# Optimization experiments

Measured on AMD Instinct MI355X. Metric: run time of the kernel, lower is better.

Reference implementation:

```python
import jax, jax.numpy as jnp
import numpy as np

EMB = 2048; H = 32; G = 8; D = 64; GS = H // G; EPS = 1e-6

def _rmsnorm(x, scale):
    x32 = x.astype(jnp.float32)
    var = jnp.mean(x32 * x32, axis=-1, keepdims=True)
    return (x32 * jax.lax.rsqrt(var + EPS) * scale).astype(x.dtype)

def _rope(x, cos, sin):
    # x: [B, h, S, D]; cos/sin: [S, D]
    d = x.shape[-1]
    x1, x2 = x[..., : d // 2], x[..., d // 2 :]
    rot = jnp.concatenate([-x2, x1], axis=-1)
    return (x * cos[None, None] + rot * sin[None, None]).astype(x.dtype)

def setup_inputs() -> dict:
    key = jax.random.key(0)
    ks = jax.random.split(key, 6)
    B, S = 2, 2048
    x = jax.random.normal(ks[0], (B, S, EMB), jnp.float32)
    # causal mask: True = blocked (masked_fill semantics)
    mask = jnp.triu(jnp.ones((S, S), dtype=bool), k=1)
    # standard RoPE tables, half-dim rotation, shape [S, D]
    inv_freq = 1.0 / (10000.0 ** (jnp.arange(0, D, 2, dtype=jnp.float32) / D))
    ang = jnp.arange(S, dtype=jnp.float32)[:, None] * inv_freq[None, :]  # [S, D/2]
    cos = jnp.concatenate([jnp.cos(ang), jnp.cos(ang)], axis=-1)
    sin = jnp.concatenate([jnp.sin(ang), jnp.sin(ang)], axis=-1)
    Wq = jax.random.normal(ks[1], (EMB, H * D), jnp.float32) * 0.02
    Wk = jax.random.normal(ks[2], (EMB, G * D), jnp.float32) * 0.02
    Wv = jax.random.normal(ks[3], (EMB, G * D), jnp.float32) * 0.02
    Wo = jax.random.normal(ks[4], (H * D, EMB), jnp.float32) * 0.02
    q_scale = jnp.ones((D,), jnp.float32)
    k_scale = jnp.ones((D,), jnp.float32)
    return {"x": x, "mask": mask, "cos": cos, "sin": sin, "Wq": Wq, "Wk": Wk,
            "Wv": Wv, "Wo": Wo, "q_scale": q_scale, "k_scale": k_scale}

def reference(x, mask, cos, sin, Wq, Wk, Wv, Wo, q_scale, k_scale):
    B, S, _ = x.shape
    q = (x @ Wq).reshape(B, S, H, D).transpose(0, 2, 1, 3)  # [B,H,S,D]
    k = (x @ Wk).reshape(B, S, G, D).transpose(0, 2, 1, 3)  # [B,G,S,D]
    v = (x @ Wv).reshape(B, S, G, D).transpose(0, 2, 1, 3)
    q = _rmsnorm(q, q_scale)
    k = _rmsnorm(k, k_scale)
    q = _rope(q, cos, sin)
    k = _rope(k, cos, sin)
    # GQA expansion (repeat_interleave over head dim)
    k = jnp.repeat(k, GS, axis=1)
    v = jnp.repeat(v, GS, axis=1)
    scale = 1.0 / np.float32(np.sqrt(D))
    s = jnp.einsum('bhqd,bhkd->bhqk', q.astype(jnp.float32), k.astype(jnp.float32)) * scale
    # flash path is causal regardless of `mask` arg; mask here equals causal
    s = jnp.where(mask[None, None], -jnp.inf, s)
    w = jax.nn.softmax(s, axis=-1)
    ctx = jnp.einsum('bhqk,bhkd->bhqd', w, v.astype(jnp.float32))
    ctx = ctx.transpose(0, 2, 1, 3).reshape(B, S, H * D)
    return ctx @ Wo
```

## Files before the change

### kernel.cpp

```cpp
#include <hip/hip_runtime.h>
#include <hip/hip_bf16.h>
#include <cstdint>
#include <cstddef>

#define EMB   2048
#define NH_   32
#define NG_   8
#define DH_   64
#define SEQ_  2048
#define BB_   2
#define MTOT  4096
#define LDQKV 3072

typedef __attribute__((ext_vector_type(8))) short s16x8;
typedef __attribute__((ext_vector_type(8))) unsigned short u16x8;
typedef __attribute__((ext_vector_type(4))) float f32x4;
typedef __attribute__((ext_vector_type(16))) float f32x16;
typedef __attribute__((ext_vector_type(4))) unsigned int u32x4;
typedef __attribute__((ext_vector_type(2))) unsigned int u32x2;
typedef __attribute__((ext_vector_type(2))) int i32x2;

__device__ __forceinline__ float bf2f(unsigned short u) {
  unsigned int x = (unsigned int)u << 16; return __uint_as_float(x);
}
__device__ __forceinline__ unsigned short f2bf(float f) {
  unsigned int x = __float_as_uint(f);
  x = x + 0x7FFFu + ((x >> 16) & 1u);
  return (unsigned short)(x >> 16);
}
__device__ __forceinline__ float ninf() { return __int_as_float(0xff800000); }
__device__ __forceinline__ unsigned int pack_bf2(float a, float b) {
  unsigned int r;
  asm("v_cvt_pk_bf16_f32 %0, %1, %2" : "=v"(r) : "v"(a), "v"(b));
  return r;
}
__device__ __forceinline__ void plswap(unsigned int& a, unsigned int& b) {
  i32x2 r = __builtin_amdgcn_permlane32_swap((int)a, (int)b, false, false);
  a = (unsigned int)r[0]; b = (unsigned int)r[1];
}
__device__ __forceinline__ void plswapf(float& a, float& b) {
  unsigned int ua = __float_as_uint(a), ub = __float_as_uint(b);
  plswap(ua, ub);
  a = __uint_as_float(ua); b = __uint_as_float(ub);
}

__device__ __forceinline__ void glds16(const void* g, void* l) {
  __builtin_amdgcn_global_load_lds((const __attribute__((address_space(1))) void*)g,
                                   (__attribute__((address_space(3))) void*)l, 16, 0, 0);
}

__global__ __launch_bounds__(256)
void cvtx(const float* __restrict__ x, unsigned short* __restrict__ xb) {
  size_t i = (size_t)blockIdx.x * 256 + threadIdx.x;
  float4 a = *(const float4*)(x + i * 8);
  float4 c = *(const float4*)(x + i * 8 + 4);
  u16x8 o;
  o[0] = f2bf(a.x); o[1] = f2bf(a.y); o[2] = f2bf(a.z); o[3] = f2bf(a.w);
  o[4] = f2bf(c.x); o[5] = f2bf(c.y); o[6] = f2bf(c.z); o[7] = f2bf(c.w);
  *(u16x8*)(xb + i * 8) = o;
}

__global__ __launch_bounds__(256)
void wtrans(const float* __restrict__ in, unsigned short* __restrict__ out, int N) {
  __shared__ float tile[64][65];
  const int tid = threadIdx.x;
  const int n0 = blockIdx.x * 64, k0 = blockIdx.y * 64;
  #pragma unroll
  for (int jj = 0; jj < 4; ++jj) {
    int r = (tid >> 4) + jj * 16;
    int c = (tid & 15) * 4;
    float4 v = *(const float4*)(in + (size_t)(k0 + r) * N + n0 + c);
    tile[r][c] = v.x; tile[r][c + 1] = v.y; tile[r][c + 2] = v.z; tile[r][c + 3] = v.w;
  }
  __syncthreads();
  #pragma unroll
  for (int rep = 0; rep < 2; ++rep) {
    int u = rep * 256 + tid;
    int nl = u >> 3, ch = u & 7;
    u16x8 o;
    #pragma unroll
    for (int e = 0; e < 8; ++e) o[e] = f2bf(tile[ch * 8 + e][nl]);
    *(u16x8*)(out + (size_t)(n0 + nl) * 2048 + k0 + ch * 8) = o;
  }
}

template<int BF16OUT>
__global__ __launch_bounds__(256)
void gemm_bt(const unsigned short* __restrict__ A, const unsigned short* __restrict__ Bt,
             void* __restrict__ C, int ldc) {
  __shared__ __align__(16) unsigned short As[128 * 32];
  __shared__ __align__(16) unsigned short Bs[128 * 32];
  const int tid = threadIdx.x;
  const int w = tid >> 6, lane = tid & 63;
  const int grp = lane >> 4, l15 = lane & 15;
  const int wr = w >> 1, wc = w & 1;
  const int bm = blockIdx.y * 128, bn = blockIdx.x * 128;
  f32x4 acc[4][4] = {};
  for (int k0 = 0; k0 < 2048; k0 += 32) {
    #pragma unroll
    for (int j = 0; j < 2; ++j) {
      int unit = (j * 4 + w) * 64 + lane;
      int row = unit >> 2, ch = unit & 3;
      glds16(A  + (size_t)(bm + row) * 2048 + k0 + ch * 8, (char*)As + (j * 4 + w) * 1024);
      glds16(Bt + (size_t)(bn + row) * 2048 + k0 + ch * 8, (char*)Bs + (j * 4 + w) * 1024);
    }
    __syncthreads();
    s16x8 af[4], bf[4];
    #pragma unroll
    for (int i = 0; i < 4; ++i)
      af[i] = *(const s16x8*)((const char*)As + (wr * 64 + i * 16 + l15) * 64 + grp * 16);
    #pragma unroll
    for (int j = 0; j < 4; ++j)
      bf[j] = *(const s16x8*)((const char*)Bs + (wc * 64 + j * 16 + l15) * 64 + grp * 16);
    #pragma unroll
    for (int i = 0; i < 4; ++i)
      #pragma unroll
      for (int j = 0; j < 4; ++j)
        acc[i][j] = __builtin_amdgcn_mfma_f32_16x16x32_bf16(af[i], bf[j], acc[i][j], 0, 0, 0);
    __syncthreads();
  }
  #pragma unroll
  for (int i = 0; i < 4; ++i)
    #pragma unroll
    for (int j = 0; j < 4; ++j)
      #pragma unroll
      for (int r = 0; r < 4; ++r) {
        int row = bm + wr * 64 + i * 16 + grp * 4 + r;
        int col = bn + wc * 64 + j * 16 + l15;
        float v = acc[i][j][r];
        if (BF16OUT) ((unsigned short*)C)[(size_t)row * ldc + col] = f2bf(v);
        else         ((float*)C)[(size_t)row * ldc + col] = v;
      }
}

__global__ __launch_bounds__(256)
void rmsrope(unsigned short* __restrict__ t, const float* __restrict__ scale,
             const float* __restrict__ cs, const float* __restrict__ sn, int coff, float post) {
  int m = blockIdx.x * 4 + (threadIdx.x >> 6);
  int h = blockIdx.y;
  int lane = threadIdx.x & 63;
  int spos = m & (SEQ_ - 1);
  unsigned short* p = t + (size_t)m * LDQKV + coff + h * 64 + lane;
  float val = bf2f(*p);
  float sq = val * val;
  #pragma unroll
  for (int off = 32; off; off >>= 1) sq += __shfl_xor(sq, off);
  float r = rsqrtf(sq * (1.f / 64.f) + 1e-6f);
  float xn = val * r * scale[lane];
  float partner = __shfl_xor(xn, 32);
  float c = cs[spos * 64 + lane], s = sn[spos * 64 + lane];
  float o = (lane < 32) ? (xn * c - partner * s) : fmaf(xn, c, partner * s);
  *p = f2bf(o * post);
}

__global__ __launch_bounds__(256)
void kvtile(const unsigned short* __restrict__ qkv, unsigned short* __restrict__ Kt,
            unsigned short* __restrict__ Vt) {
  __shared__ unsigned short Kl[32][72];
  __shared__ unsigned short Vl[32][72];
  const int tid = threadIdx.x;
  const int kt = blockIdx.x;
  const int bg = blockIdx.y;
  const int b = bg >> 3, g = bg & 7;
  {
    int row = tid >> 3, ch = tid & 7;
    u16x8 kv = *(const u16x8*)(qkv + (size_t)(b * SEQ_ + kt * 32 + row) * LDQKV + 2048 + g * 64 + ch * 8);
    #pragma unroll
    for (int e = 0; e < 8; ++e) Kl[row][ch * 8 + e] = kv[e];
    u16x8 vv = *(const u16x8*)(qkv + (size_t)(b * SEQ_ + kt * 32 + row) * LDQKV + 2560 + g * 64 + ch * 8);
    #pragma unroll
    for (int e = 0; e < 8; ++e) Vl[row][ch * 8 + e] = vv[e];
  }
  __syncthreads();
  {
    int c = tid >> 5, row = tid & 31;
    u16x8 o;
    #pragma unroll
    for (int e = 0; e < 8; ++e) o[e] = Kl[row][c * 8 + e];
    *(u16x8*)(Kt + (((size_t)(bg * 64 + kt)) << 11) + (c * 32 + row) * 8) = o;
  }
  {
    int c = tid >> 6, d = tid & 63;
    u16x8 o;
    #pragma unroll
    for (int e = 0; e < 8; ++e) o[e] = Vl[c * 8 + e][d];
    *(u16x8*)(Vt + (((size_t)(bg * 64 + kt)) << 11) + (c * 64 + d) * 8) = o;
  }
}

__global__ __launch_bounds__(256)
void attn_mfma9(const unsigned short* __restrict__ qkv, const unsigned short* __restrict__ Ktg,
                const unsigned short* __restrict__ Vtg, unsigned short* __restrict__ ctx) {
  __shared__ __align__(16) unsigned short LA[8 * 1024];
  __shared__ __align__(16) unsigned short LB[8 * 1024];
  const int tid = threadIdx.x;
  const int w = tid >> 6, lane = tid & 63;
  const int l31 = lane & 31, half = lane >> 5;
  const int bid = blockIdx.x;
  const int x8 = bid & 7, r = bid >> 3;
  const int bg = x8 + 8 * (r & 1);
  const int rr = r >> 1;
  const int slot = rr >> 4, gi = rr & 15;
  const int qt = (slot == 0) ? (63 - gi) : (slot == 1) ? gi
               : (slot == 2) ? (47 - gi) : (16 + gi);
  const int b = bg >> 3, g = bg & 7, h = g * 4 + w;
  const int qbase = qt * 32;
  const int nkt = qt + 1;
  const int nit = (nkt + 1) >> 1;

  s16x8 qf[4];
  #pragma unroll
  for (int s = 0; s < 4; ++s)
    qf[s] = *(const s16x8*)(qkv + (size_t)(b * SEQ_ + qbase + l31) * LDQKV + h * 64 + half * 8 + s * 16);

  f32x16 acc0 = {}, acc1 = {};
  float l_st = 0.f;

  const size_t tbase = ((size_t)(bg * 64)) << 11;
  const int soff = (w << 9) + lane * 8;

  auto stage = [&](unsigned short* Lb, int pi) {
    const int kt0 = 2 * pi, kt1 = 2 * pi + 1;
    glds16(Ktg + tbase + ((size_t)kt0 << 11) + soff, (char*)Lb + (w << 10));
    glds16(Vtg + tbase + ((size_t)kt0 << 11) + soff, (char*)Lb + 8192 + (w << 10));
    if (kt1 < nkt) {
      glds16(Ktg + tbase + ((size_t)kt1 << 11) + soff, (char*)Lb + 4096 + (w << 10));
      glds16(Vtg + tbase + ((size_t)kt1 << 11) + soff, (char*)Lb + 12288 + (w << 10));
    }
  };

  auto sub = [&](const char* Kb, const char* Vb, bool diag, float& lsum) {
    s16x8 KF0 = *(const s16x8*)(Kb + (((0 + half) << 5) + l31) * 16);
    s16x8 KF1 = *(const s16x8*)(Kb + (((2 + half) << 5) + l31) * 16);
    s16x8 KF2 = *(const s16x8*)(Kb + (((4 + half) << 5) + l31) * 16);
    s16x8 KF3 = *(const s16x8*)(Kb + (((6 + half) << 5) + l31) * 16);
    s16x8 vf00 = *(const s16x8*)(Vb + (((half) << 6) + l31) * 16);
    s16x8 vf01 = *(const s16x8*)(Vb + (((2 + half) << 6) + l31) * 16);
    s16x8 vf10 = *(const s16x8*)(Vb + (((half) << 6) + 32 + l31) * 16);
    s16x8 vf11 = *(const s16x8*)(Vb + (((2 + half) << 6) + 32 + l31) * 16);
    f32x16 st = {};
    __builtin_amdgcn_s_setprio(1);
    st = __builtin_amdgcn_mfma_f32_32x32x16_bf16(KF0, qf[0], st, 0, 0, 0);
    st = __builtin_amdgcn_mfma_f32_32x32x16_bf16(KF1, qf[1], st, 0, 0, 0);
    st = __builtin_amdgcn_mfma_f32_32x32x16_bf16(KF2, qf[2], st, 0, 0, 0);
    st = __builtin_amdgcn_mfma_f32_32x32x16_bf16(KF3, qf[3], st, 0, 0, 0);
    __builtin_amdgcn_s_setprio(0);
    if (diag) {
      #pragma unroll
      for (int r2 = 0; r2 < 16; ++r2) {
        int key = (r2 & 3) + 8 * (r2 >> 2) + 4 * half;
        if (key > l31) st[r2] = ninf();
      }
    }
    float p[16];
    #pragma unroll
    for (int r2 = 0; r2 < 16; ++r2) p[r2] = exp2f(st[r2]);
    float s8[8];
    #pragma unroll
    for (int r2 = 0; r2 < 8; ++r2) s8[r2] = p[r2] + p[r2 + 8];
    lsum += ((s8[0] + s8[1]) + (s8[2] + s8[3])) + ((s8[4] + s8[5]) + (s8[6] + s8[7]));
    unsigned int PK[8];
    #pragma unroll
    for (int j = 0; j < 8; ++j) PK[j] = pack_bf2(p[2 * j], p[2 * j + 1]);
    plswap(PK[0], PK[2]); plswap(PK[1], PK[3]);
    plswap(PK[4], PK[6]); plswap(PK[5], PK[7]);
    u32x4 pb0u, pb1u;
    pb0u[0] = PK[0]; pb0u[1] = PK[1]; pb0u[2] = PK[2]; pb0u[3] = PK[3];
    pb1u[0] = PK[4]; pb1u[1] = PK[5]; pb1u[2] = PK[6]; pb1u[3] = PK[7];
    s16x8 pb0 = __builtin_bit_cast(s16x8, pb0u);
    s16x8 pb1 = __builtin_bit_cast(s16x8, pb1u);
    __builtin_amdgcn_s_setprio(1);
    acc0 = __builtin_amdgcn_mfma_f32_32x32x16_bf16(vf00, pb0, acc0, 0, 0, 0);
    acc1 = __builtin_amdgcn_mfma_f32_32x32x16_bf16(vf10, pb0, acc1, 0, 0, 0);
    acc0 = __builtin_amdgcn_mfma_f32_32x32x16_bf16(vf01, pb1, acc0, 0, 0, 0);
    acc1 = __builtin_amdgcn_mfma_f32_32x32x16_bf16(vf11, pb1, acc1, 0, 0, 0);
    __builtin_amdgcn_s_setprio(0);
  };

  auto pair_body = [&](const unsigned short* Lb, int pi) {
    const int kt0 = 2 * pi, kt1 = 2 * pi + 1;
    float lsum = 0.f;
    sub((const char*)Lb, (const char*)Lb + 8192, kt0 == qt, lsum);
    if (kt1 < nkt)
      sub((const char*)Lb + 4096, (const char*)Lb + 12288, kt1 == qt, lsum);
    { float a2 = lsum, b2 = lsum; plswapf(a2, b2); lsum = a2 + b2; }
    l_st += lsum;
  };

  stage(LA, 0);
  int pi = 0;
  while (true) {
    __syncthreads();
    if (pi + 1 < nit) stage(LB, pi + 1);
    pair_body(LA, pi);
    ++pi; if (pi >= nit) break;
    __syncthreads();
    if (pi + 1 < nit) stage(LA, pi + 1);
    pair_body(LB, pi);
    ++pi; if (pi >= nit) break;
  }

  const float linv = 1.f / l_st;
  unsigned short* orow = ctx + (size_t)(b * SEQ_ + qbase + l31) * 2048 + h * 64;
  #pragma unroll
  for (int dt = 0; dt < 2; ++dt) {
    #pragma unroll
    for (int rq = 0; rq < 4; ++rq) {
      const int rr2 = rq * 4;
      const int d0 = dt * 32 + 8 * rq + 4 * half;
      float a0 = (dt ? acc1[rr2]     : acc0[rr2])     * linv;
      float a1 = (dt ? acc1[rr2 + 1] : acc0[rr2 + 1]) * linv;
      float a2 = (dt ? acc1[rr2 + 2] : acc0[rr2 + 2]) * linv;
      float a3 = (dt ? acc1[rr2 + 3] : acc0[rr2 + 3]) * linv;
      u32x2 o;
      o[0] = pack_bf2(a0, a1);
      o[1] = pack_bf2(a2, a3);
      *(u32x2*)(orow + d0) = o;
    }
  }
}

extern "C" void kernel_launch(void* const* d_in, const int* in_sizes, int n_in,
                              void* d_out, int out_size, void* d_ws, size_t ws_size,
                              hipStream_t stream) {
  const float* x  = (const float*)d_in[0];
  const float* cs = (const float*)d_in[2];
  const float* sn = (const float*)d_in[3];
  const float* Wq = (const float*)d_in[4];
  const float* Wk = (const float*)d_in[5];
  const float* Wv = (const float*)d_in[6];
  const float* Wo = (const float*)d_in[7];
  const float* qs = (const float*)d_in[8];
  const float* ks = (const float*)d_in[9];
  float* out = (float*)d_out;

  unsigned short* xb  = (unsigned short*)d_ws;
  unsigned short* Wt  = xb  + (size_t)4096 * 2048;
  unsigned short* Wot = Wt  + (size_t)3072 * 2048;
  unsigned short* qkv = Wot + (size_t)2048 * 2048;
  unsigned short* vTb = qkv + (size_t)4096 * 3072;
  unsigned short* ctx = vTb + (size_t)16 * 64 * 2048;
  unsigned short* Ktt = xb;

  cvtx<<<4096, 256, 0, stream>>>(x, xb);
  wtrans<<<dim3(32, 32), 256, 0, stream>>>(Wq, Wt, 2048);
  wtrans<<<dim3(8, 32),  256, 0, stream>>>(Wk, Wt + (size_t)2048 * 2048, 512);
  wtrans<<<dim3(8, 32),  256, 0, stream>>>(Wv, Wt + (size_t)2560 * 2048, 512);
  wtrans<<<dim3(32, 32), 256, 0, stream>>>(Wo, Wot, 2048);
  gemm_bt<1><<<dim3(24, 32), 256, 0, stream>>>(xb, Wt, qkv, 3072);
  rmsrope<<<dim3(1024, 32), 256, 0, stream>>>(qkv, qs, cs, sn, 0, 0.18033688f);
  rmsrope<<<dim3(1024, 8),  256, 0, stream>>>(qkv, ks, cs, sn, 2048, 1.0f);
  kvtile<<<dim3(64, 16), 256, 0, stream>>>(qkv, Ktt, vTb);
  attn_mfma9<<<1024, 256, 0, stream>>>(qkv, Ktt, vTb, ctx);
  gemm_bt<0><<<dim3(16, 32), 256, 0, stream>>>(ctx, Wot, out, 2048);
}
```

Measured before the change: 225.9 us.

## Replace QKV projection GEMM with 256x256-tile 4-stage global-to-LDS pipelined kernel

The QKV projection GEMM now uses a new kernel with 256x256 output tiles and 512 threads (8 waves of 128x64 each). It stages A and B directly from global memory into LDS through a 4-buffer ring, prefetching two K-steps ahead with XOR-swizzled addresses to avoid bank conflicts. MFMA sections run at raised wave priority. The larger tiles cut global traffic per FLOP and the pipeline is meant to hide load latency, but the grid shrinks to 192 blocks, which may underfill the 256 CUs, and each block needs 128KB of LDS.

```diff
diff --git a/kernel.cpp b/kernel.cpp
--- a/kernel.cpp
+++ b/kernel.cpp
@@ -82,6 +82,87 @@
     for (int e = 0; e < 8; ++e) o[e] = f2bf(tile[ch * 8 + e][nl]);
     *(u16x8*)(out + (size_t)(n0 + nl) * 2048 + k0 + ch * 8) = o;
   }
+}
+
+__global__ __launch_bounds__(512, 2)
+void gemm256(const unsigned short* __restrict__ A, const unsigned short* __restrict__ Bt,
+             unsigned short* __restrict__ C, int ldc) {
+  __shared__ __align__(16) char L[4][32768];
+  const int tid = threadIdx.x;
+  const int wid = tid >> 6, lane = tid & 63;
+  const int wm = wid >> 2, wn = wid & 3;
+  const int grp = lane >> 4, l15 = lane & 15;
+  const int bm = blockIdx.y * 256, bn = blockIdx.x * 256;
+  const int nt = 2048 / 32;
+
+  const int srow = tid >> 2;
+  const int sc = (tid & 3) ^ (srow & 3);
+  const int grp2 = grp ^ (l15 & 3);
+
+  auto stage_ht = [&](int t, int h) {
+    const unsigned short* src = (h < 2)
+      ? A  + (size_t)(bm + h * 128 + srow) * 2048 + t * 32 + sc * 8
+      : Bt + (size_t)(bn + (h - 2) * 128 + srow) * 2048 + t * 32 + sc * 8;
+    glds16(src, &L[t & 3][h * 8192 + wid * 1024]);
+  };
+
+  f32x4 acc[8][4] = {};
+
+  #pragma unroll
+  for (int h = 0; h < 4; ++h) stage_ht(0, h);
+  #pragma unroll
+  for (int h = 0; h < 4; ++h) stage_ht(1, h);
+  asm volatile("s_waitcnt vmcnt(4)" ::: "memory");
+  __builtin_amdgcn_sched_barrier(0);
+  __builtin_amdgcn_s_barrier();
+  __builtin_amdgcn_sched_barrier(0);
+
+  for (int t = 0; t < nt; ++t) {
+    const char* Ab = &L[t & 3][0]     + (size_t)(wm * 128 + l15) * 64 + grp2 * 16;
+    const char* Bb = &L[t & 3][16384] + (size_t)(wn * 64  + l15) * 64 + grp2 * 16;
+    const bool pre = (t + 2 < nt);
+    if (pre) { stage_ht(t + 2, 0); stage_ht(t + 2, 1); }
+    s16x8 bf[4], af[4];
+    #pragma unroll
+    for (int j = 0; j < 4; ++j) bf[j] = *(const s16x8*)(Bb + j * 1024);
+    #pragma unroll
+    for (int i = 0; i < 4; ++i) af[i] = *(const s16x8*)(Ab + i * 1024);
+    __builtin_amdgcn_s_setprio(1);
+    #pragma unroll
+    for (int i = 0; i < 4; ++i)
+      #pragma unroll
+      for (int j = 0; j < 4; ++j)
+        acc[i][j] = __builtin_amdgcn_mfma_f32_16x16x32_bf16(af[i], bf[j], acc[i][j], 0, 0, 0);
+    __builtin_amdgcn_s_setprio(0);
+    if (pre) { stage_ht(t + 2, 2); stage_ht(t + 2, 3); }
+    #pragma unroll
+    for (int i = 0; i < 4; ++i) af[i] = *(const s16x8*)(Ab + (4 + i) * 1024);
+    __builtin_amdgcn_s_setprio(1);
+    #pragma unroll
+    for (int i = 0; i < 4; ++i)
+      #pragma unroll
+      for (int j = 0; j < 4; ++j)
+        acc[4 + i][j] = __builtin_amdgcn_mfma_f32_16x16x32_bf16(af[i], bf[j], acc[4 + i][j], 0, 0, 0);
+    __builtin_amdgcn_s_setprio(0);
+    if (t + 1 < nt) {
+      if (pre) asm volatile("s_waitcnt vmcnt(4)" ::: "memory");
+      else     asm volatile("s_waitcnt vmcnt(0)" ::: "memory");
+      __builtin_amdgcn_sched_barrier(0);
+      __builtin_amdgcn_s_barrier();
+      __builtin_amdgcn_sched_barrier(0);
+    }
+  }
+
+  #pragma unroll
+  for (int i = 0; i < 8; ++i)
+    #pragma unroll
+    for (int j = 0; j < 4; ++j)
+      #pragma unroll
+      for (int r = 0; r < 4; ++r) {
+        int row = bm + wm * 128 + i * 16 + grp * 4 + r;
+        int col = bn + wn * 64 + j * 16 + l15;
+        C[(size_t)row * ldc + col] = f2bf(acc[i][j][r]);
+      }
 }
 
 template<int BF16OUT>
@@ -347,7 +428,7 @@
   wtrans<<<dim3(8, 32),  256, 0, stream>>>(Wk, Wt + (size_t)2048 * 2048, 512);
   wtrans<<<dim3(8, 32),  256, 0, stream>>>(Wv, Wt + (size_t)2560 * 2048, 512);
   wtrans<<<dim3(32, 32), 256, 0, stream>>>(Wo, Wot, 2048);
-  gemm_bt<1><<<dim3(24, 32), 256, 0, stream>>>(xb, Wt, qkv, 3072);
+  gemm256<<<dim3(12, 16), 512, 0, stream>>>(xb, Wt, qkv, 3072);
   rmsrope<<<dim3(1024, 32), 256, 0, stream>>>(qkv, qs, cs, sn, 0, 0.18033688f);
   rmsrope<<<dim3(1024, 8),  256, 0, stream>>>(qkv, ks, cs, sn, 2048, 1.0f);
   kvtile<<<dim3(64, 16), 256, 0, stream>>>(qkv, Ktt, vTb);
```

New measurement: 220.5 us. 1.02x faster.
